# Performance work log

Hardware: AMD Instinct MI355X
Metric: run time of the kernel (lower is better)

Reference implementation:

```python
import jax, jax.numpy as jnp
import numpy as np

DISP_W, MAT_W, CD_W = 1.0, 0.1, 0.5
CHUNK = 512


def _min_dists(a, b):
    # a: [B, Na, 3], b: [B, Nb, 3] -> per-point min squared distance [B, Na]
    B, Na, _ = a.shape
    a_chunks = jnp.swapaxes(a.reshape(B, Na // CHUNK, CHUNK, 3), 0, 1)  # [nc, B, chunk, 3]

    def body(carry, ac):  # ac: [B, chunk, 3]
        d = jnp.sum((ac[:, :, None, :] - b[:, None, :, :]) ** 2, axis=-1)  # [B, chunk, Nb]
        return carry, jnp.min(d, axis=-1)

    _, mins = jax.lax.scan(body, 0, a_chunks)  # [nc, B, chunk]
    return jnp.moveaxis(mins, 0, 1).reshape(B, Na)


def chamfer_distance(pred, target):
    min_p2t = _min_dists(pred, target)
    min_t2p = _min_dists(target, pred)
    return (min_p2t.mean(axis=1) + min_t2p.mean(axis=1)).mean()


def setup_inputs() -> dict:
    key = jax.random.key(0)
    k1, k2, k3, k4, k5 = jax.random.split(key, 5)
    B, N = 4, 8192
    return {
        "pred_disp": jax.random.normal(k1, (B, N, 3), dtype=jnp.float32),
        "pred_mat": jax.random.normal(k2, (B, 2), dtype=jnp.float32),
        "target_disp": jax.random.normal(k3, (B, N, 3), dtype=jnp.float32),
        "target_mat": jax.random.normal(k4, (B, 2), dtype=jnp.float32),
        "template": jax.random.normal(k5, (B, N, 3), dtype=jnp.float32),
    }


def reference(pred_disp, pred_mat, target_disp, target_mat, template):
    disp_loss = jnp.mean(jnp.abs(pred_disp - target_disp))
    mat_loss = jnp.mean((pred_mat - target_mat) ** 2)
    pred_pos = template + pred_disp
    target_pos = template + target_disp
    cd = chamfer_distance(pred_pos, target_pos)
    total = DISP_W * disp_loss + MAT_W * mat_loss + CD_W * cd
    return total
```

## Files before the change

### kernel.cpp

```cpp
#include <hip/hip_runtime.h>

#define DISP_W 1.0f
#define MAT_W  0.1f
#define CD_W   0.5f

typedef _Float16 half8 __attribute__((ext_vector_type(8)));
typedef float f32x16 __attribute__((ext_vector_type(16)));
typedef float f32x4  __attribute__((ext_vector_type(4)));

constexpr int BB = 4;
constexpr int NN = 8192;
constexpr int THREADS = 256;
constexpr int IB = 256;
constexpr int JR = 1024;
constexpr int NSTAGE = 2;
constexpr int NIB = NN / IB;
constexpr int NJQ = NN / (JR * NSTAGE);
constexpr int NCHUNK = JR / 32;
constexpr int NPTS = 2 * BB * NN;
constexpr int GRID = 2 * BB * NIB * NJQ;
constexpr int RSTRIDE = 36;
constexpr int NBF = NPTS / 256;
constexpr int PFT = JR / THREADS;


__global__ __launch_bounds__(256)
void build_frags(const float* __restrict__ pred_disp,
                 const float* __restrict__ target_disp,
                 const float* __restrict__ tmpl,
                 half8* __restrict__ fragA,
                 half8* __restrict__ fragBhi,
                 half8* __restrict__ fragBlo,
                 float* __restrict__ dsum_ws,
                 float* __restrict__ out)
{
    int p = blockIdx.x * 256 + threadIdx.x;
    if (p == 0) out[0] = 0.0f;
    int c = p >> 15;
    int b = (p >> 13) & (BB - 1);
    int n = p & (NN - 1);

    const float* dp = (c ? target_disp : pred_disp) + (size_t)b * NN * 3;
    const float* tp = tmpl + (size_t)b * NN * 3;

    int n3 = n * 3;
    float dx = dp[n3 + 0], dy = dp[n3 + 1], dz = dp[n3 + 2];
    float x = tp[n3 + 0] + dx;
    float y = tp[n3 + 1] + dy;
    float z = tp[n3 + 2] + dz;
    float cc = fmaf(x, x, fmaf(y, y, z * z));

    float s = 0.0f;
    if (c == 0) {
        const float* td = target_disp + (size_t)b * NN * 3;
        s = fabsf(dx - td[n3 + 0]) + fabsf(dy - td[n3 + 1]) + fabsf(dz - td[n3 + 2]);
    }

    _Float16 xh = (_Float16)x;  _Float16 xl = (_Float16)(x - (float)xh);
    _Float16 yh = (_Float16)y;  _Float16 yl = (_Float16)(y - (float)yh);
    _Float16 zh = (_Float16)z;  _Float16 zl = (_Float16)(z - (float)zh);
    _Float16 ch = (_Float16)cc; _Float16 cl = (_Float16)(cc - (float)ch);

    float ux = -2.0f * x, uy = -2.0f * y, uz = -2.0f * z;
    _Float16 uxh = (_Float16)ux; _Float16 uxl = (_Float16)(ux - (float)uxh);
    _Float16 uyh = (_Float16)uy; _Float16 uyl = (_Float16)(uy - (float)uyh);
    _Float16 uzh = (_Float16)uz; _Float16 uzl = (_Float16)(uz - (float)uzh);

    const _Float16 one  = (_Float16)1.0f;
    const _Float16 zero = (_Float16)0.0f;

    half8 aHi = {xh, yh, zh, xh, yh, zh, xl, yl};
    half8 aLo = {zl, ch, cl, one, one, zero, zero, zero};
    half8 bHi = {uxh, uyh, uzh, uxl, uyl, uzl, uxh, uyh};
    half8 bLo = {uzh, one, one, ch, cl, zero, zero, zero};

    fragA[(size_t)p * 2 + 0] = aHi;
    fragA[(size_t)p * 2 + 1] = aLo;
    fragBhi[p] = bHi;
    fragBlo[p] = bLo;

    for (int off = 32; off > 0; off >>= 1)
        s += __shfl_down(s, off, 64);
    __shared__ float ws4[4];
    int lane = threadIdx.x & 63, w = threadIdx.x >> 6;
    if (lane == 0) ws4[w] = s;
    __syncthreads();
    if (threadIdx.x == 0)
        dsum_ws[blockIdx.x] = ws4[0] + ws4[1] + ws4[2] + ws4[3];
}

__global__ __launch_bounds__(THREADS, 2)
void chamfer_mfma(const half8* __restrict__ fragA,
                  const half8* __restrict__ fragBhi,
                  const half8* __restrict__ fragBlo,
                  float* __restrict__ rowpart)
{
    __shared__ __align__(16) char lds_raw[32768];
    half8* sBhi = (half8*)lds_raw;
    half8* sBlo = (half8*)(lds_raw + 16384);

    int bx = blockIdx.x;
    int jq   = bx & (NJQ - 1);
    int iBlk = (bx >> 2) & (NIB - 1);
    int b    = (bx >> 7) & (BB - 1);
    int dir  = bx >> 9;
    int cA = dir, cB = dir ^ 1;

    const int tid  = threadIdx.x;
    const int lane = tid & 63;
    const int w    = tid >> 6;
    const int hi   = lane >> 5;
    const int li   = lane & 31;

    int i0 = iBlk * IB + w * 64 + li;
    size_t aBase = ((size_t)cA * BB + b) * NN;
    half8 aF0 = fragA[(aBase + i0) * 2 + hi];
    half8 aF1 = fragA[(aBase + i0 + 32) * 2 + hi];

    size_t pB = ((size_t)cB * BB + b) * NN + (size_t)jq * (JR * NSTAGE);
    const half8* gHi = fragBhi + pB;
    const half8* gLo = fragBlo + pB;

    f32x16 kZero = {0.f,0.f,0.f,0.f, 0.f,0.f,0.f,0.f, 0.f,0.f,0.f,0.f, 0.f,0.f,0.f,0.f};
    float rm0[16], rm1[16];
    #pragma unroll
    for (int r = 0; r < 16; ++r) { rm0[r] = 1.0e30f; rm1[r] = 1.0e30f; }

    half8 pfHi[PFT], pfLo[PFT];
    #pragma unroll
    for (int t = 0; t < PFT; ++t) {
        pfHi[t] = gHi[t * THREADS + tid];
        pfLo[t] = gLo[t * THREADS + tid];
    }
    #pragma unroll
    for (int t = 0; t < PFT; ++t) {
        sBhi[t * THREADS + tid] = pfHi[t];
        sBlo[t * THREADS + tid] = pfLo[t];
    }
    __syncthreads();

    for (int s = 0; s < NSTAGE; ++s) {
        if (s + 1 < NSTAGE) {
            const half8* srcHi = gHi + (size_t)(s + 1) * JR;
            const half8* srcLo = gLo + (size_t)(s + 1) * JR;
            #pragma unroll
            for (int t = 0; t < PFT; ++t) {
                pfHi[t] = srcHi[t * THREADS + tid];
                pfLo[t] = srcLo[t * THREADS + tid];
            }
        }

        const half8* baseB = hi ? sBlo : sBhi;
        #pragma unroll 4
        for (int c = 0; c < NCHUNK; ++c) {
            half8 b0 = baseB[c * 32 + li];
            f32x16 a0 = __builtin_amdgcn_mfma_f32_32x32x16_f16(aF0, b0, kZero, 0, 0, 0);
            f32x16 a1 = __builtin_amdgcn_mfma_f32_32x32x16_f16(aF1, b0, kZero, 0, 0, 0);
            #pragma unroll
            for (int r = 0; r < 16; ++r)
                rm0[r] = fminf(rm0[r], a0[r]);
            #pragma unroll
            for (int r = 0; r < 16; ++r)
                rm1[r] = fminf(rm1[r], a1[r]);
        }
        __syncthreads();

        if (s + 1 < NSTAGE) {
            #pragma unroll
            for (int t = 0; t < PFT; ++t) {
                sBhi[t * THREADS + tid] = pfHi[t];
                sBlo[t * THREADS + tid] = pfLo[t];
            }
            __syncthreads();
        }
    }

    float* scr = (float*)lds_raw;
    int wbase = w * (32 * RSTRIDE);
    int cbase = wbase + hi * 4 * RSTRIDE + li;
    size_t obase = ((size_t)(dir * BB + b) * NJQ + jq) * NN
                 + (size_t)iBlk * IB + w * 64;

    #pragma unroll
    for (int r = 0; r < 16; ++r)
        scr[cbase + ((r & 3) + 8 * (r >> 2)) * RSTRIDE] = rm0[r];
    __syncthreads();
    {
        const f32x4* rp = (const f32x4*)&scr[wbase + (lane & 31) * RSTRIDE];
        f32x4 q0 = rp[0], q1 = rp[1], q2 = rp[2], q3 = rp[3];
        f32x4 q4 = rp[4], q5 = rp[5], q6 = rp[6], q7 = rp[7];
        f32x4 m4;
        #pragma unroll
        for (int k = 0; k < 4; ++k)
            m4[k] = fminf(fminf(fminf(q0[k], q1[k]), fminf(q2[k], q3[k])),
                          fminf(fminf(q4[k], q5[k]), fminf(q6[k], q7[k])));
        float m = fminf(fminf(m4[0], m4[1]), fminf(m4[2], m4[3]));
        if (lane < 32) rowpart[obase + lane] = m;
    }
    __syncthreads();

    #pragma unroll
    for (int r = 0; r < 16; ++r)
        scr[cbase + ((r & 3) + 8 * (r >> 2)) * RSTRIDE] = rm1[r];
    __syncthreads();
    {
        const f32x4* rp = (const f32x4*)&scr[wbase + (lane & 31) * RSTRIDE];
        f32x4 q0 = rp[0], q1 = rp[1], q2 = rp[2], q3 = rp[3];
        f32x4 q4 = rp[4], q5 = rp[5], q6 = rp[6], q7 = rp[7];
        f32x4 m4;
        #pragma unroll
        for (int k = 0; k < 4; ++k)
            m4[k] = fminf(fminf(fminf(q0[k], q1[k]), fminf(q2[k], q3[k])),
                          fminf(fminf(q4[k], q5[k]), fminf(q6[k], q7[k])));
        float m = fminf(fminf(m4[0], m4[1]), fminf(m4[2], m4[3]));
        if (lane < 32) rowpart[obase + 32 + lane] = m;
    }
}

__global__ __launch_bounds__(256)
void final_reduce(const float* __restrict__ pred_mat,
                  const float* __restrict__ target_mat,
                  const float* __restrict__ rowpart,
                  const float* __restrict__ dsum_ws,
                  float* __restrict__ out)
{
    const int NROWS = 2 * BB * NN;

    int gtid = blockIdx.x * blockDim.x + threadIdx.x;
    int gstride = gridDim.x * blockDim.x;

    float msum = 0.0f;
    for (int t = gtid; t < NROWS; t += gstride) {
        int db = t >> 13;
        int i  = t & (NN - 1);
        const float* p = rowpart + (size_t)db * NJQ * NN + i;
        float m = 1.0e30f;
        #pragma unroll
        for (int jb = 0; jb < NJQ; ++jb)
            m = fminf(m, p[(size_t)jb * NN]);
        msum += fmaxf(m, 0.0f);
    }

    float acc = msum * (CD_W / (float)(BB * NN));

    if (gtid < NBF)
        acc += dsum_ws[gtid] * (DISP_W / (float)(BB * NN * 3));

    if (gtid < 2 * BB) {
        float d = pred_mat[gtid] - target_mat[gtid];
        acc += d * d * (MAT_W / (float)(2 * BB));
    }

    for (int off = 32; off > 0; off >>= 1)
        acc += __shfl_down(acc, off, 64);

    __shared__ float wsum[4];
    if ((threadIdx.x & 63) == 0) wsum[threadIdx.x >> 6] = acc;
    __syncthreads();
    if (threadIdx.x == 0)
        atomicAdd(out, wsum[0] + wsum[1] + wsum[2] + wsum[3]);
}

extern "C" void kernel_launch(void* const* d_in, const int* in_sizes, int n_in,
                              void* d_out, int out_size, void* d_ws, size_t ws_size,
                              hipStream_t stream) {
    const float* pred_disp   = (const float*)d_in[0];
    const float* pred_mat    = (const float*)d_in[1];
    const float* target_disp = (const float*)d_in[2];
    const float* target_mat  = (const float*)d_in[3];
    const float* tmpl        = (const float*)d_in[4];

    half8* fragA   = (half8*)d_ws;
    half8* fragBhi = fragA + (size_t)NPTS * 2;
    half8* fragBlo = fragBhi + NPTS;
    float* rowpart = (float*)(fragBlo + NPTS);
    float* dsum_ws = rowpart + (size_t)2 * BB * NJQ * NN;
    float* out = (float*)d_out;

    build_frags<<<NBF, 256, 0, stream>>>(pred_disp, target_disp, tmpl,
                                         fragA, fragBhi, fragBlo, dsum_ws, out);
    chamfer_mfma<<<GRID, THREADS, 0, stream>>>(fragA, fragBhi, fragBlo, rowpart);
    final_reduce<<<128, 256, 0, stream>>>(pred_mat, target_mat, rowpart, dsum_ws, out);
}
```

Baseline: 33.18 us.

## Compute both chamfer directions from one distance matrix via row and column mins

Instead of computing the pred→target and target→pred distance matrices separately, each block now computes one matrix tile and extracts both row minima and column minima. Column minima are reduced across the MFMA output registers and across lane halves with a shuffle, staged in LDS per wave, then written to a new colpart buffer. The final reduction combines both. This halves the MFMA work and grid size, at the cost of extra per-chunk min reductions, LDS writes and larger column partial buffers. The stage size and count are retuned (JR 512, 4 stages).

Result: slower. 43.96 us (+32.5%).

```diff
diff --git a/kernel.cpp b/kernel.cpp
--- a/kernel.cpp
+++ b/kernel.cpp
@@ -12,15 +12,16 @@
 constexpr int NN = 8192;
 constexpr int THREADS = 256;
 constexpr int IB = 256;
-constexpr int JR = 1024;
-constexpr int NSTAGE = 2;
+constexpr int JR = 512;
+constexpr int NSTAGE = 4;
+constexpr int JB = JR * NSTAGE;
 constexpr int NIB = NN / IB;
-constexpr int NJQ = NN / (JR * NSTAGE);
+constexpr int NJQ = NN / JB;
 constexpr int NCHUNK = JR / 32;
-constexpr int NPTS = 2 * BB * NN;
-constexpr int GRID = 2 * BB * NIB * NJQ;
+constexpr int NPT2 = BB * NN;
+constexpr int GRID = BB * NIB * NJQ;
 constexpr int RSTRIDE = 36;
-constexpr int NBF = NPTS / 256;
+constexpr int NBF = NPT2 / 256;
 constexpr int PFT = JR / THREADS;
 
 
@@ -36,48 +37,49 @@
 {
     int p = blockIdx.x * 256 + threadIdx.x;
     if (p == 0) out[0] = 0.0f;
-    int c = p >> 15;
-    int b = (p >> 13) & (BB - 1);
+    int b = p >> 13;
     int n = p & (NN - 1);
 
-    const float* dp = (c ? target_disp : pred_disp) + (size_t)b * NN * 3;
-    const float* tp = tmpl + (size_t)b * NN * 3;
+    const float* pd = pred_disp   + (size_t)b * NN * 3;
+    const float* td = target_disp + (size_t)b * NN * 3;
+    const float* tp = tmpl        + (size_t)b * NN * 3;
 
     int n3 = n * 3;
-    float dx = dp[n3 + 0], dy = dp[n3 + 1], dz = dp[n3 + 2];
-    float x = tp[n3 + 0] + dx;
-    float y = tp[n3 + 1] + dy;
-    float z = tp[n3 + 2] + dz;
-    float cc = fmaf(x, x, fmaf(y, y, z * z));
-
-    float s = 0.0f;
-    if (c == 0) {
-        const float* td = target_disp + (size_t)b * NN * 3;
-        s = fabsf(dx - td[n3 + 0]) + fabsf(dy - td[n3 + 1]) + fabsf(dz - td[n3 + 2]);
-    }
-
-    _Float16 xh = (_Float16)x;  _Float16 xl = (_Float16)(x - (float)xh);
-    _Float16 yh = (_Float16)y;  _Float16 yl = (_Float16)(y - (float)yh);
-    _Float16 zh = (_Float16)z;  _Float16 zl = (_Float16)(z - (float)zh);
-    _Float16 ch = (_Float16)cc; _Float16 cl = (_Float16)(cc - (float)ch);
-
-    float ux = -2.0f * x, uy = -2.0f * y, uz = -2.0f * z;
-    _Float16 uxh = (_Float16)ux; _Float16 uxl = (_Float16)(ux - (float)uxh);
-    _Float16 uyh = (_Float16)uy; _Float16 uyl = (_Float16)(uy - (float)uyh);
-    _Float16 uzh = (_Float16)uz; _Float16 uzl = (_Float16)(uz - (float)uzh);
+    float pdx = pd[n3 + 0], pdy = pd[n3 + 1], pdz = pd[n3 + 2];
+    float tdx = td[n3 + 0], tdy = td[n3 + 1], tdz = td[n3 + 2];
+    float t0 = tp[n3 + 0], t1 = tp[n3 + 1], t2 = tp[n3 + 2];
+
+    float s = fabsf(pdx - tdx) + fabsf(pdy - tdy) + fabsf(pdz - tdz);
 
     const _Float16 one  = (_Float16)1.0f;
     const _Float16 zero = (_Float16)0.0f;
 
-    half8 aHi = {xh, yh, zh, xh, yh, zh, xl, yl};
-    half8 aLo = {zl, ch, cl, one, one, zero, zero, zero};
-    half8 bHi = {uxh, uyh, uzh, uxl, uyl, uzl, uxh, uyh};
-    half8 bLo = {uzh, one, one, ch, cl, zero, zero, zero};
-
-    fragA[(size_t)p * 2 + 0] = aHi;
-    fragA[(size_t)p * 2 + 1] = aLo;
-    fragBhi[p] = bHi;
-    fragBlo[p] = bLo;
+    {
+        float x = t0 + pdx, y = t1 + pdy, z = t2 + pdz;
+        float cc = fmaf(x, x, fmaf(y, y, z * z));
+        _Float16 xh = (_Float16)x;  _Float16 xl = (_Float16)(x - (float)xh);
+        _Float16 yh = (_Float16)y;  _Float16 yl = (_Float16)(y - (float)yh);
+        _Float16 zh = (_Float16)z;  _Float16 zl = (_Float16)(z - (float)zh);
+        _Float16 ch = (_Float16)cc; _Float16 cl = (_Float16)(cc - (float)ch);
+        half8 aHi = {xh, yh, zh, xh, yh, zh, xl, yl};
+        half8 aLo = {zl, ch, cl, one, one, zero, zero, zero};
+        fragA[(size_t)p * 2 + 0] = aHi;
+        fragA[(size_t)p * 2 + 1] = aLo;
+    }
+
+    {
+        float x = t0 + tdx, y = t1 + tdy, z = t2 + tdz;
+        float cc = fmaf(x, x, fmaf(y, y, z * z));
+        float ux = -2.0f * x, uy = -2.0f * y, uz = -2.0f * z;
+        _Float16 uxh = (_Float16)ux; _Float16 uxl = (_Float16)(ux - (float)uxh);
+        _Float16 uyh = (_Float16)uy; _Float16 uyl = (_Float16)(uy - (float)uyh);
+        _Float16 uzh = (_Float16)uz; _Float16 uzl = (_Float16)(uz - (float)uzh);
+        _Float16 ch = (_Float16)cc; _Float16 cl = (_Float16)(cc - (float)ch);
+        half8 bHi = {uxh, uyh, uzh, uxl, uyl, uzl, uxh, uyh};
+        half8 bLo = {uzh, one, one, ch, cl, zero, zero, zero};
+        fragBhi[p] = bHi;
+        fragBlo[p] = bLo;
+    }
 
     for (int off = 32; off > 0; off >>= 1)
         s += __shfl_down(s, off, 64);
@@ -93,18 +95,18 @@
 void chamfer_mfma(const half8* __restrict__ fragA,
                   const half8* __restrict__ fragBhi,
                   const half8* __restrict__ fragBlo,
-                  float* __restrict__ rowpart)
+                  float* __restrict__ rowpart,
+                  float* __restrict__ colpart)
 {
-    __shared__ __align__(16) char lds_raw[32768];
+    __shared__ __align__(16) char lds_raw[49152];
     half8* sBhi = (half8*)lds_raw;
-    half8* sBlo = (half8*)(lds_raw + 16384);
+    half8* sBlo = (half8*)(lds_raw + 8192);
+    float* colw = (float*)(lds_raw + 16384);
 
     int bx = blockIdx.x;
     int jq   = bx & (NJQ - 1);
     int iBlk = (bx >> 2) & (NIB - 1);
-    int b    = (bx >> 7) & (BB - 1);
-    int dir  = bx >> 9;
-    int cA = dir, cB = dir ^ 1;
+    int b    = bx >> 7;
 
     const int tid  = threadIdx.x;
     const int lane = tid & 63;
@@ -113,11 +115,11 @@
     const int li   = lane & 31;
 
     int i0 = iBlk * IB + w * 64 + li;
-    size_t aBase = ((size_t)cA * BB + b) * NN;
+    size_t aBase = (size_t)b * NN;
     half8 aF0 = fragA[(aBase + i0) * 2 + hi];
     half8 aF1 = fragA[(aBase + i0 + 32) * 2 + hi];
 
-    size_t pB = ((size_t)cB * BB + b) * NN + (size_t)jq * (JR * NSTAGE);
+    size_t pB = (size_t)b * NN + (size_t)jq * JB;
     const half8* gHi = fragBhi + pB;
     const half8* gLo = fragBlo + pB;
 
@@ -151,6 +153,7 @@
         }
 
         const half8* baseB = hi ? sBlo : sBhi;
+        const int cwBase = w * JB + s * JR;
         #pragma unroll 4
         for (int c = 0; c < NCHUNK; ++c) {
             half8 b0 = baseB[c * 32 + li];
@@ -162,6 +165,15 @@
             #pragma unroll
             for (int r = 0; r < 16; ++r)
                 rm1[r] = fminf(rm1[r], a1[r]);
+            float cv[16];
+            #pragma unroll
+            for (int r = 0; r < 16; ++r) cv[r] = fminf(a0[r], a1[r]);
+            #pragma unroll
+            for (int st = 8; st > 0; st >>= 1)
+                #pragma unroll
+                for (int r = 0; r < st; ++r) cv[r] = fminf(cv[r], cv[r + st]);
+            float v = fminf(cv[0], __shfl_xor(cv[0], 32, 64));
+            if (lane < 32) colw[cwBase + c * 32 + lane] = v;
         }
         __syncthreads();
 
@@ -175,11 +187,18 @@
         }
     }
 
-    float* scr = (float*)lds_raw;
+    size_t cpBase = ((size_t)b * NIB + iBlk) * NN + (size_t)jq * JB;
+    for (int j = tid; j < JB; j += THREADS) {
+        float v = fminf(fminf(colw[j], colw[JB + j]),
+                        fminf(colw[2 * JB + j], colw[3 * JB + j]));
+        colpart[cpBase + j] = v;
+    }
+    __syncthreads();
+
+    float* scr = (float*)(lds_raw + 16384);
     int wbase = w * (32 * RSTRIDE);
     int cbase = wbase + hi * 4 * RSTRIDE + li;
-    size_t obase = ((size_t)(dir * BB + b) * NJQ + jq) * NN
-                 + (size_t)iBlk * IB + w * 64;
+    size_t obase = ((size_t)b * NJQ + jq) * NN + (size_t)iBlk * IB + w * 64;
 
     #pragma unroll
     for (int r = 0; r < 16; ++r)
@@ -221,24 +240,29 @@
 void final_reduce(const float* __restrict__ pred_mat,
                   const float* __restrict__ target_mat,
                   const float* __restrict__ rowpart,
+                  const float* __restrict__ colpart,
                   const float* __restrict__ dsum_ws,
                   float* __restrict__ out)
 {
-    const int NROWS = 2 * BB * NN;
-
     int gtid = blockIdx.x * blockDim.x + threadIdx.x;
     int gstride = gridDim.x * blockDim.x;
 
     float msum = 0.0f;
-    for (int t = gtid; t < NROWS; t += gstride) {
-        int db = t >> 13;
-        int i  = t & (NN - 1);
-        const float* p = rowpart + (size_t)db * NJQ * NN + i;
-        float m = 1.0e30f;
+    for (int t = gtid; t < NPT2; t += gstride) {
+        int b = t >> 13;
+        int i = t & (NN - 1);
+        const float* rp = rowpart + (size_t)b * NJQ * NN + i;
+        float mr = 1.0e30f;
         #pragma unroll
         for (int jb = 0; jb < NJQ; ++jb)
-            m = fminf(m, p[(size_t)jb * NN]);
-        msum += fmaxf(m, 0.0f);
+            mr = fminf(mr, rp[(size_t)jb * NN]);
+        msum += fmaxf(mr, 0.0f);
+        const float* cp = colpart + (size_t)b * NIB * NN + i;
+        float mc = 1.0e30f;
+        #pragma unroll 8
+        for (int ib = 0; ib < NIB; ++ib)
+            mc = fminf(mc, cp[(size_t)ib * NN]);
+        msum += fmaxf(mc, 0.0f);
     }
 
     float acc = msum * (CD_W / (float)(BB * NN));
@@ -271,14 +295,17 @@
     const float* tmpl        = (const float*)d_in[4];
 
     half8* fragA   = (half8*)d_ws;
-    half8* fragBhi = fragA + (size_t)NPTS * 2;
-    half8* fragBlo = fragBhi + NPTS;
-    float* rowpart = (float*)(fragBlo + NPTS);
-    float* dsum_ws = rowpart + (size_t)2 * BB * NJQ * NN;
+    half8* fragBhi = fragA + (size_t)NPT2 * 2;
+    half8* fragBlo = fragBhi + NPT2;
+    float* rowpart = (float*)(fragBlo + NPT2);
+    float* colpart = rowpart + (size_t)BB * NJQ * NN;
+    float* dsum_ws = colpart + (size_t)BB * NIB * NN;
     float* out = (float*)d_out;
 
     build_frags<<<NBF, 256, 0, stream>>>(pred_disp, target_disp, tmpl,
                                          fragA, fragBhi, fragBlo, dsum_ws, out);
-    chamfer_mfma<<<GRID, THREADS, 0, stream>>>(fragA, fragBhi, fragBlo, rowpart);
-    final_reduce<<<128, 256, 0, stream>>>(pred_mat, target_mat, rowpart, dsum_ws, out);
+    chamfer_mfma<<<GRID, THREADS, 0, stream>>>(fragA, fragBhi, fragBlo,
+                                               rowpart, colpart);
+    final_reduce<<<128, 256, 0, stream>>>(pred_mat, target_mat, rowpart, colpart,
+                                          dsum_ws, out);
 }
```
